# Kernel optimization log

Measured on AMD Instinct MI355X. Metric: run time of the kernel, lower is better.

The kernel has to match this reference:

```python
import jax, jax.numpy as jnp
import numpy as np

# Module constants from Net.__init__
KS = (3, 8, 2)          # kernel_size per pseudo-coordinate dim
K = KS[0] * KS[1] * KS[2]  # 48 spline weight matrices per layer
DIM = 3
S = 2 ** DIM            # 8 nonzero degree-1 B-spline supports per edge
MAX_RADIUS = 4.5
N, E = 20000, 500000


def _glorot(key, shape):
    fan = shape[-2] + shape[-1]
    return jax.random.normal(key, shape, jnp.float32) * jnp.sqrt(2.0 / fan)


def setup_inputs() -> dict:
    key = jax.random.key(0)
    ks = jax.random.split(key, 12)
    x = jax.random.normal(ks[0], (N, 1), jnp.float32)
    edge_index = jax.random.randint(ks[1], (2, E), 0, N)
    # raw pseudo-coordinates in [0, max_radius); normalized inside reference
    pseudo = jax.random.uniform(ks[2], (E, DIM), jnp.float32) * MAX_RADIUS
    return {
        "x": x,
        "edge_index": edge_index,
        "pseudo": pseudo,
        "W1": _glorot(ks[3], (K, 1, 32)),   "root1": _glorot(ks[4], (1, 32)),   "b1": jnp.zeros((32,), jnp.float32),
        "W2": _glorot(ks[5], (K, 32, 64)),  "root2": _glorot(ks[6], (32, 64)),  "b2": jnp.zeros((64,), jnp.float32),
        "W3": _glorot(ks[7], (K, 64, 128)), "root3": _glorot(ks[8], (64, 128)), "b3": jnp.zeros((128,), jnp.float32),
    }


def spline_basis(u):
    """Degree-1 open B-spline basis. u: [E, DIM] in [0,1].
    Returns basis [E, S] and flat kernel indices kidx [E, S] into the K weights."""
    ks_f = jnp.array(KS, jnp.float32)
    pos = u * (ks_f - 1.0)                      # [E, DIM]
    lo = jnp.floor(pos)
    frac = pos - lo                             # interpolation weight per dim
    lo_i = lo.astype(jnp.int32)
    # all 2^DIM corner offsets
    bits = jnp.array([[(s >> d) & 1 for d in range(DIM)] for s in range(S)], jnp.int32)  # [S, DIM]
    idx = jnp.clip(lo_i[:, None, :] + bits[None, :, :], 0, jnp.array(KS, jnp.int32) - 1)  # [E, S, DIM]
    w = jnp.where(bits[None, :, :] == 1, frac[:, None, :], 1.0 - frac[:, None, :])        # [E, S, DIM]
    basis = jnp.prod(w, axis=-1)                # [E, S]
    strides = jnp.array([KS[1] * KS[2], KS[2], 1], jnp.int32)
    kidx = (idx * strides[None, None, :]).sum(-1)  # [E, S]
    return basis, kidx


def spline_conv(x, src, dst, basis, kidx, W, root, bias):
    """SplineGCN layer: gather source features, weight by spline basis,
    scatter-add into per-(node, kernel) buckets, then contract with the K
    kernel matrices. Equivalent to sum_e basis * (x_src @ W[kidx]) at dst."""
    c_in = x.shape[1]
    contrib = basis[:, :, None] * x[src][:, None, :]          # [E, S, c_in]
    flat = (dst[:, None] * K + kidx).reshape(-1)              # [E*S]
    acc = jax.ops.segment_sum(contrib.reshape(-1, c_in), flat, num_segments=N * K)
    acc = acc.reshape(N, K, c_in)                             # [N, K, c_in]
    return jnp.einsum('nki,kio->no', acc, W) + x @ root + bias


def reference(x, edge_index, pseudo, W1, root1, b1, W2, root2, b2, W3, root3, b3):
    u = jnp.clip(pseudo / MAX_RADIUS, 0.0, 1.0)
    basis, kidx = spline_basis(u)
    src, dst = edge_index[0], edge_index[1]
    h = jax.nn.relu(spline_conv(x, src, dst, basis, kidx, W1, root1, b1))
    h = jax.nn.relu(spline_conv(h, src, dst, basis, kidx, W2, root2, b2))
    h = jax.nn.relu(spline_conv(h, src, dst, basis, kidx, W3, root3, b3))
    return jax.nn.log_softmax(h, axis=-1)
```

## Files before the change

kernel.cpp:

```cpp
#include <hip/hip_runtime.h>
#include <hip/hip_bf16.h>

#define NN_NODES 20000
#define NE_EDGES 500000
#define KTOT 48
#define BTSTRIDE 40

typedef __bf16 bf16x8 __attribute__((ext_vector_type(8)));
typedef float f32x4 __attribute__((ext_vector_type(4)));

__device__ inline unsigned short bf16_rne(float x) {
    unsigned int u = __float_as_uint(x);
    u = (u + 0x7fffu + ((u >> 16) & 1u)) >> 16;
    return (unsigned short)u;
}

__global__ void zero_kernel(int* __restrict__ p, int n) {
    int i = blockIdx.x * 256 + threadIdx.x;
    if (i < n) p[i] = 0;
}

__global__ void count_kernel(const int* __restrict__ ei, int* __restrict__ counts) {
    int e = blockIdx.x * 256 + threadIdx.x;
    if (e < NE_EDGES) atomicAdd(&counts[ei[NE_EDGES + e]], 1);
}

__global__ void scan_kernel(const int* __restrict__ counts, int* __restrict__ row_start) {
    __shared__ int part[256];
    const int CH = (NN_NODES + 255) / 256;
    int t = threadIdx.x;
    int begin = t * CH;
    int end = begin + CH;
    if (end > NN_NODES) end = NN_NODES;
    int sum = 0;
    for (int i = begin; i < end && i < NN_NODES; ++i) sum += counts[i];
    part[t] = sum;
    __syncthreads();
    for (int off = 1; off < 256; off <<= 1) {
        int v = (t >= off) ? part[t - off] : 0;
        __syncthreads();
        part[t] += v;
        __syncthreads();
    }
    int run = (t == 0) ? 0 : part[t - 1];
    for (int i = begin; i < end && i < NN_NODES; ++i) {
        row_start[i] = run;
        run += counts[i];
    }
    if (t == 255) row_start[NN_NODES] = part[255];
}

__global__ void fill_kernel(const int* __restrict__ ei, const int* __restrict__ row_start,
                            int* __restrict__ cursor, int* __restrict__ slot_pos) {
    int e = blockIdx.x * 256 + threadIdx.x;
    if (e < NE_EDGES) {
        int d = ei[NE_EDGES + e];
        int p = atomicAdd(&cursor[d], 1);
        slot_pos[e] = row_start[d] + p;
    }
}

__global__ void edge_prep_sorted(const float* __restrict__ pseudo, const int* __restrict__ ei,
                                 const int* __restrict__ slot_pos,
                                 int* __restrict__ srcs,
                                 float* __restrict__ bas8, unsigned char* __restrict__ kidb) {
    int e = blockIdx.x * 256 + threadIdx.x;
    if (e >= NE_EDGES) return;
    const int ksa[3] = {3, 8, 2};
    float frac[3];
    int id_lo[3], id_hi[3];
#pragma unroll
    for (int d = 0; d < 3; ++d) {
        float u = pseudo[e * 3 + d] * (1.0f / 4.5f);
        u = fminf(fmaxf(u, 0.0f), 1.0f);
        float pos = u * (float)(ksa[d] - 1);
        float fl = floorf(pos);
        int lo = (int)fl;
        frac[d] = pos - fl;
        id_lo[d] = lo;
        id_hi[d] = (lo + 1 <= ksa[d] - 1) ? lo + 1 : lo - 1;
    }
    int j = slot_pos[e];
    srcs[j] = ei[e];
#pragma unroll
    for (int s = 0; s < 8; ++s) {
        float w = 1.0f;
        int k = 0;
        const int strides[3] = {16, 2, 1};
#pragma unroll
        for (int d = 0; d < 3; ++d) {
            int bit = (s >> d) & 1;
            k += (bit ? id_hi[d] : id_lo[d]) * strides[d];
            w *= bit ? frac[d] : (1.0f - frac[d]);
        }
        bas8[(size_t)j * 8 + s] = w;
        kidb[(size_t)j * 8 + s] = (unsigned char)k;
    }
}

__global__ __launch_bounds__(256) void layer1_fused_kernel(
    const int* __restrict__ srcs, const float* __restrict__ bas8,
    const unsigned char* __restrict__ kidb, const int* __restrict__ row_start,
    const float* __restrict__ x, const float* __restrict__ W1,
    const float* __restrict__ root1, const float* __restrict__ b1,
    unsigned short* __restrict__ h1bf) {
    __shared__ float w1s[KTOT * 32];
    __shared__ float scopy[4][8 * 49];
    int tid = threadIdx.x;
    for (int l = tid; l < KTOT * 32; l += 256) w1s[l] = W1[l];
    int w = tid >> 6, lane = tid & 63;
    int n = blockIdx.x * 4 + w;
    bool act = n < NN_NODES;
    float* sc = &scopy[w][0];
    for (int l = lane; l < 8 * 49; l += 64) sc[l] = 0.0f;
    if (act) {
        int beg = row_start[n], end = row_start[n + 1];
        int es = lane >> 3;
        for (int jb = beg; jb < end; jb += 8) {
            int j = jb + es;
            if (j < end) {
                float b = bas8[(size_t)jb * 8 + lane];
                int k = kidb[(size_t)jb * 8 + lane];
                float xv = x[srcs[j]];
                sc[es * 49 + k] += b * xv;
            }
        }
        if (lane < KTOT) {
            float a = 0.0f;
#pragma unroll
            for (int e = 0; e < 8; ++e) a += sc[e * 49 + lane];
            sc[lane] = a;
        }
    }
    __syncthreads();
    if (act && lane < 32) {
        float s = b1[lane] + x[n] * root1[lane];
#pragma unroll 8
        for (int k = 0; k < KTOT; ++k) s = fmaf(sc[k], w1s[k * 32 + lane], s);
        h1bf[n * 32 + lane] = bf16_rne(fmaxf(s, 0.0f));
    }
}

__global__ void pack_w_kernel(const float* __restrict__ W, const float* __restrict__ root,
                              int KK, int NN, int total, unsigned short* __restrict__ Wp) {
    int tid = blockIdx.x * 256 + threadIdx.x;
    if (tid >= total) return;
    int nct = NN >> 4;
    int l = tid & 63;
    int c = (tid >> 6) % nct;
    int t = tid / (64 * nct);
    int n = c * 16 + (l & 15);
    int kbase = t * 32 + ((l >> 4) << 3);
    unsigned short vals[8];
#pragma unroll
    for (int jj = 0; jj < 8; ++jj) {
        int k = kbase + jj;
        float v = (k < KK) ? W[(size_t)k * NN + n] : root[(size_t)(k - KK) * NN + n];
        vals[jj] = bf16_rne(v);
    }
    *(uint4*)&Wp[(size_t)tid * 8] = *(uint4*)vals;
}

#define ASTR2 1576
__global__ __launch_bounds__(1024) void fused_l2_kernel(
    const int* __restrict__ srcs, const float* __restrict__ bas8,
    const unsigned char* __restrict__ kidb, const int* __restrict__ row_start,
    const unsigned short* __restrict__ h1bf, const unsigned short* __restrict__ Wp2,
    const float* __restrict__ b2, unsigned short* __restrict__ h2bf) {
    __shared__ unsigned short Arows[16 * ASTR2];
    __shared__ unsigned short BtAll[16][KTOT * BTSTRIDE];
    float* Cst = (float*)&BtAll[0][0];
    int w = threadIdx.x >> 6, lane = threadIdx.x & 63;
    int q = lane >> 4, l15 = lane & 15;
    unsigned short* Bt = &BtAll[w][0];

    {
        int n = blockIdx.x * 16 + w;
        int beg = row_start[n], end = row_start[n + 1];
        int cnt = end - beg;
        f32x4 acc[3][2] = {};
        for (int c0 = 0; c0 < cnt; c0 += 32) {
            uint4 z = make_uint4(0, 0, 0, 0);
            for (int l = lane; l < (KTOT * BTSTRIDE) / 8; l += 64) ((uint4*)Bt)[l] = z;
#pragma unroll
            for (int it = 0; it < 4; ++it) {
                int idx = it * 64 + lane;
                int jj = idx >> 3, s = idx & 7;
                int j = c0 + jj;
                if (j < cnt) {
                    float b = bas8[(size_t)(beg + j) * 8 + s];
                    int k = kidb[(size_t)(beg + j) * 8 + s];
                    Bt[k * BTSTRIDE + jj] = bf16_rne(b);
                }
            }
            int srcv[8];
#pragma unroll
            for (int j = 0; j < 8; ++j) {
                int jc = c0 + q * 8 + j;
                jc = (jc < cnt) ? jc : (cnt - 1);
                srcv[j] = srcs[beg + jc];
            }
            bf16x8 afr[3];
#pragma unroll
            for (int mt = 0; mt < 3; ++mt) {
                uint4 raw = *(const uint4*)&Bt[(mt * 16 + l15) * BTSTRIDE + q * 8];
                afr[mt] = __builtin_bit_cast(bf16x8, raw);
            }
#pragma unroll
            for (int nt = 0; nt < 2; ++nt) {
                unsigned int bw[4];
#pragma unroll
                for (int jp = 0; jp < 4; ++jp) {
                    unsigned int lo = h1bf[(size_t)srcv[2 * jp] * 32 + nt * 16 + l15];
                    unsigned int hi = h1bf[(size_t)srcv[2 * jp + 1] * 32 + nt * 16 + l15];
                    bw[jp] = lo | (hi << 16);
                }
                uint4 braw = make_uint4(bw[0], bw[1], bw[2], bw[3]);
                bf16x8 bfr = __builtin_bit_cast(bf16x8, braw);
#pragma unroll
                for (int mt = 0; mt < 3; ++mt)
                    acc[mt][nt] = __builtin_amdgcn_mfma_f32_16x16x32_bf16(
                        afr[mt], bfr, acc[mt][nt], 0, 0, 0);
            }
        }
        unsigned short* arow = &Arows[w * ASTR2];
#pragma unroll
        for (int mt = 0; mt < 3; ++mt)
#pragma unroll
            for (int nt = 0; nt < 2; ++nt)
#pragma unroll
                for (int r = 0; r < 4; ++r)
                    arow[(mt * 16 + q * 4 + r) * 32 + nt * 16 + l15] =
                        bf16_rne(acc[mt][nt][r]);
        if (lane < 32) arow[1536 + lane] = h1bf[(size_t)n * 32 + lane];
    }
    __syncthreads();

    {
        int tile = w & 3;
        int kq = w >> 2;
        int t0 = (kq * 49) / 4, t1 = ((kq + 1) * 49) / 4;
        f32x4 cacc = {};
        const uint4* wpq = (const uint4*)Wp2;
        uint4 nb = wpq[((size_t)t0 * 4 + tile) * 64 + lane];
        for (int t = t0; t < t1; ++t) {
            uint4 cb = nb;
            int tn = (t + 1 < t1) ? t + 1 : t;
            nb = wpq[((size_t)tn * 4 + tile) * 64 + lane];
            bf16x8 af = __builtin_bit_cast(
                bf16x8, *(const uint4*)&Arows[l15 * ASTR2 + t * 32 + (q << 3)]);
            bf16x8 bfr = __builtin_bit_cast(bf16x8, cb);
            cacc = __builtin_amdgcn_mfma_f32_16x16x32_bf16(af, bfr, cacc, 0, 0, 0);
        }
        float* cpart = Cst + kq * (16 * 66);
#pragma unroll
        for (int r = 0; r < 4; ++r)
            cpart[(q * 4 + r) * 66 + tile * 16 + l15] = cacc[r];
    }
    __syncthreads();

    {
        int row = threadIdx.x >> 6;
        int col = threadIdx.x & 63;
        int idx = row * 66 + col;
        float v = Cst[idx] + Cst[16 * 66 + idx] + Cst[32 * 66 + idx] + Cst[48 * 66 + idx];
        v = fmaxf(v + b2[col], 0.0f);
        int n = blockIdx.x * 16 + row;
        h2bf[(size_t)n * 64 + col] = bf16_rne(v);
    }
}

#define ASTR 3160
__global__ __launch_bounds__(1024) void fused_l3_kernel(
    const int* __restrict__ srcs, const float* __restrict__ bas8,
    const unsigned char* __restrict__ kidb, const int* __restrict__ row_start,
    const unsigned short* __restrict__ h2bf, const unsigned short* __restrict__ Wp3,
    const float* __restrict__ b3, float* __restrict__ out) {
    __shared__ unsigned short Arows[16 * ASTR];
    __shared__ unsigned short BtAll[16][KTOT * BTSTRIDE];
    float* Cst = (float*)&BtAll[0][0];
    int w = threadIdx.x >> 6, lane = threadIdx.x & 63;
    int q = lane >> 4, l15 = lane & 15;
    unsigned short* Bt = &BtAll[w][0];

    {
        int n = blockIdx.x * 16 + w;
        int beg = row_start[n], end = row_start[n + 1];
        int cnt = end - beg;
        f32x4 acc[3][4] = {};
        for (int c0 = 0; c0 < cnt; c0 += 32) {
            uint4 z = make_uint4(0, 0, 0, 0);
            for (int l = lane; l < (KTOT * BTSTRIDE) / 8; l += 64) ((uint4*)Bt)[l] = z;
#pragma unroll
            for (int it = 0; it < 4; ++it) {
                int idx = it * 64 + lane;
                int jj = idx >> 3, s = idx & 7;
                int j = c0 + jj;
                if (j < cnt) {
                    float b = bas8[(size_t)(beg + j) * 8 + s];
                    int k = kidb[(size_t)(beg + j) * 8 + s];
                    Bt[k * BTSTRIDE + jj] = bf16_rne(b);
                }
            }
            int srcv[8];
#pragma unroll
            for (int j = 0; j < 8; ++j) {
                int jc = c0 + q * 8 + j;
                jc = (jc < cnt) ? jc : (cnt - 1);
                srcv[j] = srcs[beg + jc];
            }
            bf16x8 afr[3];
#pragma unroll
            for (int mt = 0; mt < 3; ++mt) {
                uint4 raw = *(const uint4*)&Bt[(mt * 16 + l15) * BTSTRIDE + q * 8];
                afr[mt] = __builtin_bit_cast(bf16x8, raw);
            }
#pragma unroll
            for (int nt = 0; nt < 4; ++nt) {
                unsigned int bw[4];
#pragma unroll
                for (int jp = 0; jp < 4; ++jp) {
                    unsigned int lo = h2bf[(size_t)srcv[2 * jp] * 64 + nt * 16 + l15];
                    unsigned int hi = h2bf[(size_t)srcv[2 * jp + 1] * 64 + nt * 16 + l15];
                    bw[jp] = lo | (hi << 16);
                }
                uint4 braw = make_uint4(bw[0], bw[1], bw[2], bw[3]);
                bf16x8 bfr = __builtin_bit_cast(bf16x8, braw);
#pragma unroll
                for (int mt = 0; mt < 3; ++mt)
                    acc[mt][nt] = __builtin_amdgcn_mfma_f32_16x16x32_bf16(
                        afr[mt], bfr, acc[mt][nt], 0, 0, 0);
            }
        }
        unsigned short* arow = &Arows[w * ASTR];
#pragma unroll
        for (int mt = 0; mt < 3; ++mt)
#pragma unroll
            for (int nt = 0; nt < 4; ++nt)
#pragma unroll
                for (int r = 0; r < 4; ++r)
                    arow[(mt * 16 + q * 4 + r) * 64 + nt * 16 + l15] =
                        bf16_rne(acc[mt][nt][r]);
        arow[3072 + lane] = h2bf[(size_t)(blockIdx.x * 16 + w) * 64 + lane];
    }
    __syncthreads();

    {
        int tile = w & 7;
        int half = w >> 3;
        int t0 = half * 49, t1 = t0 + 49;
        f32x4 cacc = {};
        const uint4* wpq = (const uint4*)Wp3;
        uint4 nb = wpq[((size_t)t0 * 8 + tile) * 64 + lane];
        for (int t = t0; t < t1; ++t) {
            uint4 cb = nb;
            int tn = (t + 1 < t1) ? t + 1 : t;
            nb = wpq[((size_t)tn * 8 + tile) * 64 + lane];
            bf16x8 af = __builtin_bit_cast(
                bf16x8, *(const uint4*)&Arows[l15 * ASTR + t * 32 + (q << 3)]);
            bf16x8 bfr = __builtin_bit_cast(bf16x8, cb);
            cacc = __builtin_amdgcn_mfma_f32_16x16x32_bf16(af, bfr, cacc, 0, 0, 0);
        }
        float* chalf = Cst + half * (16 * 130);
#pragma unroll
        for (int r = 0; r < 4; ++r)
            chalf[(q * 4 + r) * 130 + tile * 16 + l15] = cacc[r];
    }
    __syncthreads();

    if (threadIdx.x < 256) {
        int row = threadIdx.x >> 4;
        int cb0 = threadIdx.x & 15;
        float v[8];
        float mx = -1e30f;
#pragma unroll
        for (int c = 0; c < 8; ++c) {
            int idx = row * 130 + cb0 + c * 16;
            float s = Cst[idx] + Cst[16 * 130 + idx] + b3[cb0 + c * 16];
            s = fmaxf(s, 0.0f);
            v[c] = s;
            mx = fmaxf(mx, s);
        }
#pragma unroll
        for (int off = 8; off > 0; off >>= 1) mx = fmaxf(mx, __shfl_xor(mx, off));
        float se = 0.0f;
#pragma unroll
        for (int c = 0; c < 8; ++c) se += expf(v[c] - mx);
#pragma unroll
        for (int off = 8; off > 0; off >>= 1) se += __shfl_xor(se, off);
        float lse = mx + logf(se);
        int n = blockIdx.x * 16 + row;
#pragma unroll
        for (int c = 0; c < 8; ++c)
            out[(size_t)n * 128 + cb0 + c * 16] = v[c] - lse;
    }
}

extern "C" void kernel_launch(void* const* d_in, const int* in_sizes, int n_in,
                              void* d_out, int out_size, void* d_ws, size_t ws_size,
                              hipStream_t stream) {
    const float* x = (const float*)d_in[0];
    const int* ei = (const int*)d_in[1];
    const float* pseudo = (const float*)d_in[2];
    const float* W1 = (const float*)d_in[3];
    const float* root1 = (const float*)d_in[4];
    const float* b1 = (const float*)d_in[5];
    const float* W2 = (const float*)d_in[6];
    const float* root2 = (const float*)d_in[7];
    const float* b2 = (const float*)d_in[8];
    const float* W3 = (const float*)d_in[9];
    const float* root3 = (const float*)d_in[10];
    const float* b3 = (const float*)d_in[11];
    float* out = (float*)d_out;
    char* ws = (char*)d_ws;

    const int N = NN_NODES, E = NE_EDGES;
    const int Kp2 = 49 * 32;
    const int Kp3 = 49 * 64;
    size_t off = 0;
    auto carve = [&](size_t bytes) {
        size_t p = off;
        off += (bytes + 255) & ~(size_t)255;
        return p;
    };
    int* counts = (int*)(ws + carve((size_t)N * 4 * 2));
    int* cursor = counts + N;
    int* row_start = (int*)(ws + carve((size_t)(N + 1) * 4));
    int* slot_pos = (int*)(ws + carve((size_t)E * 4));
    int* srcs = (int*)(ws + carve((size_t)E * 4));
    float* bas8 = (float*)(ws + carve((size_t)E * 8 * 4));
    unsigned char* kidb = (unsigned char*)(ws + carve((size_t)E * 8));
    unsigned short* h1bf = (unsigned short*)(ws + carve((size_t)N * 32 * 2));
    unsigned short* h2bf = (unsigned short*)(ws + carve((size_t)N * 64 * 2));
    unsigned short* Wp2 = (unsigned short*)(ws + carve((size_t)Kp2 * 64 * 2));
    unsigned short* Wp3 = (unsigned short*)(ws + carve((size_t)Kp3 * 128 * 2));

    int egrid = (E + 255) / 256;

    zero_kernel<<<(2 * N + 255) / 256, 256, 0, stream>>>(counts, 2 * N);
    count_kernel<<<egrid, 256, 0, stream>>>(ei, counts);
    scan_kernel<<<1, 256, 0, stream>>>(counts, row_start);
    fill_kernel<<<egrid, 256, 0, stream>>>(ei, row_start, cursor, slot_pos);
    edge_prep_sorted<<<egrid, 256, 0, stream>>>(pseudo, ei, slot_pos, srcs, bas8, kidb);

    int tot2 = (Kp2 / 32) * (64 / 16) * 64;
    int tot3 = (Kp3 / 32) * (128 / 16) * 64;
    pack_w_kernel<<<(tot2 + 255) / 256, 256, 0, stream>>>(W2, root2, KTOT * 32, 64, tot2, Wp2);
    pack_w_kernel<<<(tot3 + 255) / 256, 256, 0, stream>>>(W3, root3, KTOT * 64, 128, tot3, Wp3);

    layer1_fused_kernel<<<(N + 3) / 4, 256, 0, stream>>>(srcs, bas8, kidb, row_start, x,
                                                         W1, root1, b1, h1bf);

    fused_l2_kernel<<<N / 16, 1024, 0, stream>>>(srcs, bas8, kidb, row_start,
                                                 h1bf, Wp2, b2, h2bf);

    fused_l3_kernel<<<N / 16, 1024, 0, stream>>>(srcs, bas8, kidb, row_start,
                                                 h2bf, Wp3, b3, out);
}
```

Baseline: 307.2 us.

## Fuse CSR fill into edge prep, store basis as bf16, pad/swizzle LDS rows

Merges the slot-assignment atomic kernel into edge_prep_sorted, which drops one launch and the slot_pos buffer round trip. Spline basis values are now stored as bf16 instead of fp32, halving that stream's traffic. Layer 1 reads them back by widening to float, so its accumulation now sees bf16-rounded weights. Layer-2 LDS rows are padded to stride 36 and layer-3 LDS rows get an XOR swizzle, both meant to reduce bank conflicts on the MFMA A-fragment loads.

```diff
diff --git a/kernel.cpp b/kernel.cpp
--- a/kernel.cpp
+++ b/kernel.cpp
@@ -50,20 +50,11 @@
     if (t == 255) row_start[NN_NODES] = part[255];
 }
 
-__global__ void fill_kernel(const int* __restrict__ ei, const int* __restrict__ row_start,
-                            int* __restrict__ cursor, int* __restrict__ slot_pos) {
-    int e = blockIdx.x * 256 + threadIdx.x;
-    if (e < NE_EDGES) {
-        int d = ei[NE_EDGES + e];
-        int p = atomicAdd(&cursor[d], 1);
-        slot_pos[e] = row_start[d] + p;
-    }
-}
-
 __global__ void edge_prep_sorted(const float* __restrict__ pseudo, const int* __restrict__ ei,
-                                 const int* __restrict__ slot_pos,
+                                 const int* __restrict__ row_start, int* __restrict__ cursor,
                                  int* __restrict__ srcs,
-                                 float* __restrict__ bas8, unsigned char* __restrict__ kidb) {
+                                 unsigned short* __restrict__ bas8bf,
+                                 unsigned char* __restrict__ kidb) {
     int e = blockIdx.x * 256 + threadIdx.x;
     if (e >= NE_EDGES) return;
     const int ksa[3] = {3, 8, 2};
@@ -80,7 +71,9 @@
         id_lo[d] = lo;
         id_hi[d] = (lo + 1 <= ksa[d] - 1) ? lo + 1 : lo - 1;
     }
-    int j = slot_pos[e];
+    int d0 = ei[NE_EDGES + e];
+    int p = atomicAdd(&cursor[d0], 1);
+    int j = row_start[d0] + p;
     srcs[j] = ei[e];
 #pragma unroll
     for (int s = 0; s < 8; ++s) {
@@ -93,13 +86,13 @@
             k += (bit ? id_hi[d] : id_lo[d]) * strides[d];
             w *= bit ? frac[d] : (1.0f - frac[d]);
         }
-        bas8[(size_t)j * 8 + s] = w;
+        bas8bf[(size_t)j * 8 + s] = bf16_rne(w);
         kidb[(size_t)j * 8 + s] = (unsigned char)k;
     }
 }
 
 __global__ __launch_bounds__(256) void layer1_fused_kernel(
-    const int* __restrict__ srcs, const float* __restrict__ bas8,
+    const int* __restrict__ srcs, const unsigned short* __restrict__ bas8bf,
     const unsigned char* __restrict__ kidb, const int* __restrict__ row_start,
     const float* __restrict__ x, const float* __restrict__ W1,
     const float* __restrict__ root1, const float* __restrict__ b1,
@@ -119,7 +112,7 @@
         for (int jb = beg; jb < end; jb += 8) {
             int j = jb + es;
             if (j < end) {
-                float b = bas8[(size_t)jb * 8 + lane];
+                float b = __uint_as_float((unsigned)bas8bf[(size_t)jb * 8 + lane] << 16);
                 int k = kidb[(size_t)jb * 8 + lane];
                 float xv = x[srcs[j]];
                 sc[es * 49 + k] += b * xv;
@@ -161,13 +154,13 @@
     *(uint4*)&Wp[(size_t)tid * 8] = *(uint4*)vals;
 }
 
-#define ASTR2 1576
+#define NSTR2 1816
 __global__ __launch_bounds__(1024) void fused_l2_kernel(
-    const int* __restrict__ srcs, const float* __restrict__ bas8,
+    const int* __restrict__ srcs, const unsigned short* __restrict__ bas8bf,
     const unsigned char* __restrict__ kidb, const int* __restrict__ row_start,
     const unsigned short* __restrict__ h1bf, const unsigned short* __restrict__ Wp2,
     const float* __restrict__ b2, unsigned short* __restrict__ h2bf) {
-    __shared__ unsigned short Arows[16 * ASTR2];
+    __shared__ unsigned short Arows[16 * NSTR2];
     __shared__ unsigned short BtAll[16][KTOT * BTSTRIDE];
     float* Cst = (float*)&BtAll[0][0];
     int w = threadIdx.x >> 6, lane = threadIdx.x & 63;
@@ -188,9 +181,9 @@
                 int jj = idx >> 3, s = idx & 7;
                 int j = c0 + jj;
                 if (j < cnt) {
-                    float b = bas8[(size_t)(beg + j) * 8 + s];
+                    unsigned short b = bas8bf[(size_t)(beg + j) * 8 + s];
                     int k = kidb[(size_t)(beg + j) * 8 + s];
-                    Bt[k * BTSTRIDE + jj] = bf16_rne(b);
+                    Bt[k * BTSTRIDE + jj] = b;
                 }
             }
             int srcv[8];
@@ -223,16 +216,16 @@
                         afr[mt], bfr, acc[mt][nt], 0, 0, 0);
             }
         }
-        unsigned short* arow = &Arows[w * ASTR2];
+        unsigned short* arow = &Arows[w * NSTR2];
 #pragma unroll
         for (int mt = 0; mt < 3; ++mt)
 #pragma unroll
             for (int nt = 0; nt < 2; ++nt)
 #pragma unroll
                 for (int r = 0; r < 4; ++r)
-                    arow[(mt * 16 + q * 4 + r) * 32 + nt * 16 + l15] =
+                    arow[(mt * 16 + q * 4 + r) * 36 + nt * 16 + l15] =
                         bf16_rne(acc[mt][nt][r]);
-        if (lane < 32) arow[1536 + lane] = h1bf[(size_t)n * 32 + lane];
+        if (lane < 32) arow[48 * 36 + lane] = h1bf[(size_t)n * 32 + lane];
     }
     __syncthreads();
 
@@ -248,7 +241,7 @@
             int tn = (t + 1 < t1) ? t + 1 : t;
             nb = wpq[((size_t)tn * 4 + tile) * 64 + lane];
             bf16x8 af = __builtin_bit_cast(
-                bf16x8, *(const uint4*)&Arows[l15 * ASTR2 + t * 32 + (q << 3)]);
+                bf16x8, *(const uint4*)&Arows[l15 * NSTR2 + t * 36 + (q << 3)]);
             bf16x8 bfr = __builtin_bit_cast(bf16x8, cb);
             cacc = __builtin_amdgcn_mfma_f32_16x16x32_bf16(af, bfr, cacc, 0, 0, 0);
         }
@@ -272,7 +265,7 @@
 
 #define ASTR 3160
 __global__ __launch_bounds__(1024) void fused_l3_kernel(
-    const int* __restrict__ srcs, const float* __restrict__ bas8,
+    const int* __restrict__ srcs, const unsigned short* __restrict__ bas8bf,
     const unsigned char* __restrict__ kidb, const int* __restrict__ row_start,
     const unsigned short* __restrict__ h2bf, const unsigned short* __restrict__ Wp3,
     const float* __restrict__ b3, float* __restrict__ out) {
@@ -297,9 +290,9 @@
                 int jj = idx >> 3, s = idx & 7;
                 int j = c0 + jj;
                 if (j < cnt) {
-                    float b = bas8[(size_t)(beg + j) * 8 + s];
+                    unsigned short b = bas8bf[(size_t)(beg + j) * 8 + s];
                     int k = kidb[(size_t)(beg + j) * 8 + s];
-                    Bt[k * BTSTRIDE + jj] = bf16_rne(b);
+                    Bt[k * BTSTRIDE + jj] = b;
                 }
             }
             int srcv[8];
@@ -333,13 +326,14 @@
             }
         }
         unsigned short* arow = &Arows[w * ASTR];
+        int sw = q << 4;
 #pragma unroll
         for (int mt = 0; mt < 3; ++mt)
 #pragma unroll
             for (int nt = 0; nt < 4; ++nt)
 #pragma unroll
                 for (int r = 0; r < 4; ++r)
-                    arow[(mt * 16 + q * 4 + r) * 64 + nt * 16 + l15] =
+                    arow[(mt * 16 + q * 4 + r) * 64 + ((nt * 16 + l15) ^ sw)] =
                         bf16_rne(acc[mt][nt][r]);
         arow[3072 + lane] = h2bf[(size_t)(blockIdx.x * 16 + w) * 64 + lane];
     }
@@ -356,8 +350,11 @@
             uint4 cb = nb;
             int tn = (t + 1 < t1) ? t + 1 : t;
             nb = wpq[((size_t)tn * 8 + tile) * 64 + lane];
+            int kk = t >> 1;
+            int chb = ((t & 1) << 5) + (q << 3);
+            int sw = ((kk >> 2) & 3) << 4;
             bf16x8 af = __builtin_bit_cast(
-                bf16x8, *(const uint4*)&Arows[l15 * ASTR + t * 32 + (q << 3)]);
+                bf16x8, *(const uint4*)&Arows[l15 * ASTR + kk * 64 + (chb ^ sw)]);
             bf16x8 bfr = __builtin_bit_cast(bf16x8, cb);
             cacc = __builtin_amdgcn_mfma_f32_16x16x32_bf16(af, bfr, cacc, 0, 0, 0);
         }
@@ -426,9 +423,8 @@
     int* counts = (int*)(ws + carve((size_t)N * 4 * 2));
     int* cursor = counts + N;
     int* row_start = (int*)(ws + carve((size_t)(N + 1) * 4));
-    int* slot_pos = (int*)(ws + carve((size_t)E * 4));
     int* srcs = (int*)(ws + carve((size_t)E * 4));
-    float* bas8 = (float*)(ws + carve((size_t)E * 8 * 4));
+    unsigned short* bas8bf = (unsigned short*)(ws + carve((size_t)E * 8 * 2));
     unsigned char* kidb = (unsigned char*)(ws + carve((size_t)E * 8));
     unsigned short* h1bf = (unsigned short*)(ws + carve((size_t)N * 32 * 2));
     unsigned short* h2bf = (unsigned short*)(ws + carve((size_t)N * 64 * 2));
@@ -440,20 +436,20 @@
     zero_kernel<<<(2 * N + 255) / 256, 256, 0, stream>>>(counts, 2 * N);
     count_kernel<<<egrid, 256, 0, stream>>>(ei, counts);
     scan_kernel<<<1, 256, 0, stream>>>(counts, row_start);
-    fill_kernel<<<egrid, 256, 0, stream>>>(ei, row_start, cursor, slot_pos);
-    edge_prep_sorted<<<egrid, 256, 0, stream>>>(pseudo, ei, slot_pos, srcs, bas8, kidb);
+    edge_prep_sorted<<<egrid, 256, 0, stream>>>(pseudo, ei, row_start, cursor,
+                                                srcs, bas8bf, kidb);
 
     int tot2 = (Kp2 / 32) * (64 / 16) * 64;
     int tot3 = (Kp3 / 32) * (128 / 16) * 64;
     pack_w_kernel<<<(tot2 + 255) / 256, 256, 0, stream>>>(W2, root2, KTOT * 32, 64, tot2, Wp2);
     pack_w_kernel<<<(tot3 + 255) / 256, 256, 0, stream>>>(W3, root3, KTOT * 64, 128, tot3, Wp3);
 
-    layer1_fused_kernel<<<(N + 3) / 4, 256, 0, stream>>>(srcs, bas8, kidb, row_start, x,
+    layer1_fused_kernel<<<(N + 3) / 4, 256, 0, stream>>>(srcs, bas8bf, kidb, row_start, x,
                                                          W1, root1, b1, h1bf);
 
-    fused_l2_kernel<<<N / 16, 1024, 0, stream>>>(srcs, bas8, kidb, row_start,
+    fused_l2_kernel<<<N / 16, 1024, 0, stream>>>(srcs, bas8bf, kidb, row_start,
                                                  h1bf, Wp2, b2, h2bf);
 
-    fused_l3_kernel<<<N / 16, 1024, 0, stream>>>(srcs, bas8, kidb, row_start,
+    fused_l3_kernel<<<N / 16, 1024, 0, stream>>>(srcs, bas8bf, kidb, row_start,
                                                  h2bf, Wp3, b3, out);
 }
```

Measured after the change: 294.2 us. 1.04x faster.
